# Kernel tuning notes

Measured on AMD Instinct MI355X. Metric: run time of the kernel, lower is better.

## Reference

```python
import jax, jax.numpy as jnp
import numpy as np

NUM_LABELS = [3, 5, 8, 12, 16, 20, 24, 28, 32, 36, 40, 44, 48, 52, 58, 64]
B = 524288


def setup_inputs() -> dict:
    key = jax.random.key(0)
    k_in, k_ids, k_w = jax.random.split(key, 3)
    lengths = jnp.asarray([n - 1 for n in NUM_LABELS], dtype=jnp.int32)  # [T]
    T = len(NUM_LABELS)
    Cmax = int(max(NUM_LABELS)) - 1
    inp = jax.random.normal(k_in, (B, 1), dtype=jnp.float32)
    cutoff_ids = jax.random.randint(k_ids, (B,), 0, T, dtype=jnp.int32)
    # Padded cutoff table: per-task sorted (as in reset_parameters), padding zeroed.
    w = jnp.sort(jax.random.normal(k_w, (T, Cmax), dtype=jnp.float32), axis=-1)
    valid = jnp.arange(Cmax, dtype=jnp.int32)[None, :] < lengths[:, None]  # [T, Cmax]
    weights = jnp.where(valid, w, 0.0)
    return {"input": inp, "cutoff_ids": cutoff_ids, "weights": weights, "lengths": lengths}


def reference(input, cutoff_ids, weights, lengths):
    # Ragged nested tensors represented as padded [B, Cmax] + mask.
    pos = weights[cutoff_ids]                       # [B, Cmax] gather of per-task cutoffs
    Cmax = weights.shape[1]
    mask = jnp.arange(Cmax, dtype=lengths.dtype)[None, :] < lengths[cutoff_ids][:, None]
    # repeated_hiddens + neg_cutoffs == input[:, 0] broadcast minus cutoffs (valid slots only)
    diff = jnp.where(mask, input[:, 0:1] - pos, 0.0)  # [B, Cmax]
    pos = jnp.where(mask, pos, 0.0)
    return diff, pos
```

## Files before the change

kernel.cpp:

```cpp
#include <hip/hip_runtime.h>


#define CMAX 63
#define NTASK 16

__global__ __launch_bounds__(256) void moc_kernel(
    const float* __restrict__ inp,
    const int* __restrict__ ids,
    const float* __restrict__ weights,
    const int* __restrict__ lengths,
    float* __restrict__ out_diff,
    float* __restrict__ out_pos,
    int total)
{
    __shared__ float w_lds[NTASK * CMAX];
    __shared__ int   len_lds[NTASK];
    for (int i = threadIdx.x; i < NTASK * CMAX; i += blockDim.x)
        w_lds[i] = weights[i];
    if (threadIdx.x < NTASK)
        len_lds[threadIdx.x] = lengths[threadIdx.x];
    __syncthreads();

    const int nvec = total >> 2;
    const int stride = gridDim.x * blockDim.x;
    for (int v = blockIdx.x * blockDim.x + threadIdx.x; v < nvec; v += stride) {
        const int base = v << 2;
        float4 dv, pv;
        float* dvp = &dv.x;
        float* pvp = &pv.x;
#pragma unroll
        for (int j = 0; j < 4; ++j) {
            const int idx = base + j;
            const int b = idx / CMAX;
            const int c = idx - b * CMAX;
            const int t = ids[b];
            const float x = inp[b];
            const float w = w_lds[t * CMAX + c];
            const bool valid = c < len_lds[t];
            dvp[j] = valid ? (x - w) : 0.0f;
            pvp[j] = valid ? w : 0.0f;
        }
        reinterpret_cast<float4*>(out_diff)[v] = dv;
        reinterpret_cast<float4*>(out_pos)[v]  = pv;
    }
}

extern "C" void kernel_launch(void* const* d_in, const int* in_sizes, int n_in,
                              void* d_out, int out_size, void* d_ws, size_t ws_size,
                              hipStream_t stream) {
    const float* inp     = (const float*)d_in[0];
    const int*   ids     = (const int*)d_in[1];
    const float* weights = (const float*)d_in[2];
    const int*   lengths = (const int*)d_in[3];

    const int B = in_sizes[0];
    const int total = B * CMAX;
    float* out_diff = (float*)d_out;
    float* out_pos  = (float*)d_out + total;

    const int block = 256;
    const int grid = 2048;
    moc_kernel<<<grid, block, 0, stream>>>(inp, ids, weights, lengths,
                                           out_diff, out_pos, total);
}
```

Baseline: 44.78 us.

## Stage per-row inputs in LDS with one block per 256-row tile

Replaces the grid-stride loop with one block per 256 rows. Each thread loads its row's id, input value and length into shared memory once, so the inner loop no longer issues repeated global gathers of ids and inp for every output element. The grid becomes B/256 blocks, so every block reloads the weight table and there are more block launches. The tail handling assumes B is a multiple of 256 and has no bounds check on the output.

```diff
diff --git a/kernel.cpp b/kernel.cpp
--- a/kernel.cpp
+++ b/kernel.cpp
@@ -3,6 +3,9 @@
 
 #define CMAX 63
 #define NTASK 16
+#define ROWS_PER_BLOCK 256
+#define ELEMS_PER_BLOCK (ROWS_PER_BLOCK * CMAX)
+#define VECS_PER_BLOCK (ELEMS_PER_BLOCK / 4)
 
 __global__ __launch_bounds__(256) void moc_kernel(
     const float* __restrict__ inp,
@@ -11,37 +14,51 @@
     const int* __restrict__ lengths,
     float* __restrict__ out_diff,
     float* __restrict__ out_pos,
-    int total)
+    int B)
 {
     __shared__ float w_lds[NTASK * CMAX];
-    __shared__ int   len_lds[NTASK];
-    for (int i = threadIdx.x; i < NTASK * CMAX; i += blockDim.x)
+    __shared__ float x_lds[ROWS_PER_BLOCK];
+    __shared__ int   t_lds[ROWS_PER_BLOCK];
+    __shared__ int   len_lds[ROWS_PER_BLOCK];
+
+    const int tid = threadIdx.x;
+
+    for (int i = tid; i < NTASK * CMAX; i += ROWS_PER_BLOCK)
         w_lds[i] = weights[i];
-    if (threadIdx.x < NTASK)
-        len_lds[threadIdx.x] = lengths[threadIdx.x];
+
+    const int row = blockIdx.x * ROWS_PER_BLOCK + tid;
+    if (row < B) {
+        const int t = ids[row];
+        x_lds[tid]   = inp[row];
+        t_lds[tid]   = t;
+        len_lds[tid] = lengths[t];
+    }
     __syncthreads();
 
-    const int nvec = total >> 2;
-    const int stride = gridDim.x * blockDim.x;
-    for (int v = blockIdx.x * blockDim.x + threadIdx.x; v < nvec; v += stride) {
-        const int base = v << 2;
+    const int ebase = blockIdx.x * ELEMS_PER_BLOCK;
+    float4* __restrict__ od = reinterpret_cast<float4*>(out_diff + ebase);
+    float4* __restrict__ op = reinterpret_cast<float4*>(out_pos + ebase);
+
+    for (int v = tid; v < VECS_PER_BLOCK; v += ROWS_PER_BLOCK) {
+        const int lbase = v << 2;
         float4 dv, pv;
         float* dvp = &dv.x;
         float* pvp = &pv.x;
 #pragma unroll
         for (int j = 0; j < 4; ++j) {
-            const int idx = base + j;
-            const int b = idx / CMAX;
-            const int c = idx - b * CMAX;
-            const int t = ids[b];
-            const float x = inp[b];
-            const float w = w_lds[t * CMAX + c];
-            const bool valid = c < len_lds[t];
+            const int li = lbase + j;
+            const int bl = li / CMAX;
+            const int c  = li - bl * CMAX;
+            const float x   = x_lds[bl];
+            const int   t   = t_lds[bl];
+            const int   len = len_lds[bl];
+            const float w   = w_lds[t * CMAX + c];
+            const bool valid = c < len;
             dvp[j] = valid ? (x - w) : 0.0f;
             pvp[j] = valid ? w : 0.0f;
         }
-        reinterpret_cast<float4*>(out_diff)[v] = dv;
-        reinterpret_cast<float4*>(out_pos)[v]  = pv;
+        od[v] = dv;
+        op[v] = pv;
     }
 }
 
@@ -58,8 +75,7 @@
     float* out_diff = (float*)d_out;
     float* out_pos  = (float*)d_out + total;
 
-    const int block = 256;
-    const int grid = 2048;
-    moc_kernel<<<grid, block, 0, stream>>>(inp, ids, weights, lengths,
-                                           out_diff, out_pos, total);
+    const int grid = (B + ROWS_PER_BLOCK - 1) / ROWS_PER_BLOCK;
+    moc_kernel<<<grid, ROWS_PER_BLOCK, 0, stream>>>(inp, ids, weights, lengths,
+                                                    out_diff, out_pos, B);
 }
```

Result: faster. 43.10 us (median of 2 runs) (-3.7%).
